# Kernel optimization log

Measured on AMD Instinct MI355X. Metric: run time of the kernel, lower is better.

The kernel has to match this reference:

```python
import math
import jax, jax.numpy as jnp
import numpy as np

B, T, DIM, H = 2, 2048, 2048, 16
D = DIM // H  # head_dim = 128


def setup_inputs() -> dict:
    key = jax.random.key(0)
    ks = jax.random.split(key, 6)
    s = 0.02
    x = jax.random.normal(ks[0], (B, T, DIM), dtype=jnp.float32)
    # causal mask: True = keep, False = masked (matches masked_fill(mask==0, -inf))
    attn_mask = jnp.tril(jnp.ones((T, T), dtype=bool))[None, None, :, :]
    Wq = jax.random.normal(ks[1], (DIM, DIM), dtype=jnp.float32) * s
    Wk = jax.random.normal(ks[2], (DIM, D), dtype=jnp.float32) * s
    Wv = jax.random.normal(ks[3], (DIM, D), dtype=jnp.float32) * s
    Wo = jax.random.normal(ks[4], (DIM, DIM), dtype=jnp.float32) * s
    return {
        "x": x, "attn_mask": attn_mask,
        "Wq": Wq, "bq": jnp.zeros((DIM,), jnp.float32),
        "Wk": Wk, "bk": jnp.zeros((D,), jnp.float32),
        "Wv": Wv, "bv": jnp.zeros((D,), jnp.float32),
        "Wo": Wo, "bo": jnp.zeros((DIM,), jnp.float32),
    }


def _rope_freqs(t_len, d):
    inv_freq = 1.0 / (10000.0 ** (jnp.arange(0, d, 2, dtype=jnp.float32) / d))
    f = jnp.arange(t_len, dtype=jnp.float32)[:, None] * inv_freq[None, :]  # [T, d/2]
    # duplicate to full head dim so cos/sin align with rotate_half's half split
    cos = jnp.concatenate([jnp.cos(f), jnp.cos(f)], axis=-1)[None, None]  # [1,1,T,d]
    sin = jnp.concatenate([jnp.sin(f), jnp.sin(f)], axis=-1)[None, None]
    return cos, sin


def _rotate_half(u):
    d2 = u.shape[-1] // 2
    return jnp.concatenate([-u[..., d2:], u[..., :d2]], axis=-1)


def reference(x, attn_mask, Wq, bq, Wk, bk, Wv, bv, Wo, bo):
    Bx, Tx, C = x.shape
    q = (x @ Wq + bq).reshape(Bx, Tx, H, D).transpose(0, 2, 1, 3)  # [B,H,T,D]
    k = (x @ Wk + bk)[:, None]  # [B,1,T,D] single shared KV head (MQA)
    v = (x @ Wv + bv)[:, None]
    cos, sin = _rope_freqs(Tx, D)
    q = q * cos + _rotate_half(q) * sin
    k = k * cos + _rotate_half(k) * sin
    attn = jnp.matmul(q, k.swapaxes(-2, -1)) / math.sqrt(D)  # [B,H,T,T]
    attn = jnp.where(attn_mask, attn, jnp.float32(-jnp.inf))
    attn = jax.nn.softmax(attn, axis=-1)
    out = jnp.matmul(attn, v)  # [B,H,T,D]
    out = out.transpose(0, 2, 1, 3).reshape(Bx, Tx, C)
    return out @ Wo + bo
```

## Files before the change

kernel.cpp:

```cpp
#include <hip/hip_runtime.h>

typedef unsigned short u16;
typedef unsigned int u32;
typedef __bf16 bf16x8 __attribute__((ext_vector_type(8)));
typedef float f32x4 __attribute__((ext_vector_type(4)));
typedef float f32x16 __attribute__((ext_vector_type(16)));
typedef u32 u32x4 __attribute__((ext_vector_type(4)));

__device__ __forceinline__ u16 bfu(float x) {
  union { __bf16 h; u16 u; } z; z.h = (__bf16)x; return z.u;
}
__device__ __forceinline__ u32 pk2(float a, float b) {
  union { __bf16 h[2]; u32 u; } z;
  z.h[0] = (__bf16)a; z.h[1] = (__bf16)b;
  return z.u;
}
__device__ __forceinline__ void gl_lds16(const u16* g, u16* l) {
  __builtin_amdgcn_global_load_lds((const __attribute__((address_space(1))) void*)g,
                                   (__attribute__((address_space(3))) void*)l, 16, 0, 0);
}

__global__ __launch_bounds__(256) void cvt_bf16(const float* __restrict__ src, u16* __restrict__ dst, int n8) {
  int i = blockIdx.x * 256 + threadIdx.x;
  if (i >= n8) return;
  const float4* s4 = (const float4*)src;
  float4 a = s4[2 * i], b = s4[2 * i + 1];
  u32x4 o;
  o[0] = pk2(a.x, a.y); o[1] = pk2(a.z, a.w);
  o[2] = pk2(b.x, b.y); o[3] = pk2(b.z, b.w);
  ((u32x4*)dst)[i] = o;
}

__global__ void transpose_cvt(const float* __restrict__ src, u16* __restrict__ dst, int R, int C) {
  __shared__ float tile[32][33];
  const int c0 = blockIdx.x * 32, r0 = blockIdx.y * 32;
  const int tx = threadIdx.x, ty = threadIdx.y;
#pragma unroll
  for (int i = 0; i < 4; ++i)
    tile[ty + i * 8][tx] = src[(size_t)(r0 + ty + i * 8) * C + c0 + tx];
  __syncthreads();
#pragma unroll
  for (int i = 0; i < 4; ++i)
    dst[(size_t)(c0 + ty + i * 8) * R + r0 + tx] = bfu(tile[tx][ty + i * 8]);
}

__global__ void transpose_v(const float* __restrict__ QKV, const float* __restrict__ bv, u16* __restrict__ Vt) {
  __shared__ float tile[32][33];
  const int t0 = blockIdx.x * 32, d0 = blockIdx.y * 32, b = blockIdx.z;
  const int tx = threadIdx.x, ty = threadIdx.y;
#pragma unroll
  for (int i = 0; i < 4; ++i)
    tile[ty + i * 8][tx] = QKV[(size_t)(b * 2048 + t0 + ty + i * 8) * 2304 + 2176 + d0 + tx] + bv[d0 + tx];
  __syncthreads();
#pragma unroll
  for (int i = 0; i < 4; ++i)
    Vt[(size_t)b * 262144 + (size_t)(d0 + ty + i * 8) * 2048 + t0 + tx] = bfu(tile[tx][ty + i * 8]);
}

__global__ __launch_bounds__(256) void rope_qk(const float* __restrict__ QKV, const float* __restrict__ bq,
                                               const float* __restrict__ bk,
                                               u16* __restrict__ Qb, u16* __restrict__ Kb) {
  const int row = blockIdx.x;
  const int b = row >> 11, t = row & 2047;
  const int tid = threadIdx.x;
  const float* qrow = QKV + (size_t)row * 2304;
  const float scale = 0.1275173862437171f;
  const float nl2 = -0.20762050593046f;
#pragma unroll
  for (int it = 0; it < 4; ++it) {
    int idx = tid + it * 256;
    int h = idx >> 6, j = idx & 63;
    float q0 = qrow[h * 128 + j] + bq[h * 128 + j];
    float q1 = qrow[h * 128 + j + 64] + bq[h * 128 + j + 64];
    float ang = (float)t * exp2f((float)j * nl2);
    float s = sinf(ang), c = cosf(ang);
    size_t o = ((size_t)((b * 16 + h) * 2048 + t)) * 128 + j;
    Qb[o]      = bfu((q0 * c - q1 * s) * scale);
    Qb[o + 64] = bfu((q1 * c + q0 * s) * scale);
  }
  if (tid < 64) {
    int j = tid;
    float k0 = qrow[2048 + j] + bk[j];
    float k1 = qrow[2048 + j + 64] + bk[j + 64];
    float ang = (float)t * exp2f((float)j * nl2);
    float s = sinf(ang), c = cosf(ang);
    size_t o = (size_t)row * 128 + j;
    Kb[o]      = bfu(k0 * c - k1 * s);
    Kb[o + 64] = bfu(k1 * c + k0 * s);
  }
}

template <bool BIAS>
__global__ __launch_bounds__(256) void gemm_bt(const u16* __restrict__ A, const u16* __restrict__ Bt,
                                               const float* __restrict__ bias, float* __restrict__ C,
                                               int M, int N, int K) {
  const int n0 = blockIdx.x * 128, m0 = blockIdx.y * 128;
  const int tid = threadIdx.x, lane = tid & 63;
  const int wid = tid >> 6, wr = wid >> 1, wc = wid & 1;
  __shared__ __align__(16) u16 As[128 * 32];
  __shared__ __align__(16) u16 Bs[128 * 32];
  f32x4 acc[4][4];
#pragma unroll
  for (int i = 0; i < 4; ++i)
#pragma unroll
    for (int j = 0; j < 4; ++j)
#pragma unroll
      for (int rr = 0; rr < 4; ++rr) acc[i][j][rr] = 0.f;

  const int c0 = tid, c1 = tid + 256;
  const int ar0 = c0 >> 2, ac0 = (c0 & 3) * 8;
  const int ar1 = c1 >> 2, ac1 = (c1 & 3) * 8;
  const int r = lane & 15, g = lane >> 4;

  for (int k0 = 0; k0 < K; k0 += 32) {
    gl_lds16(A + (size_t)(m0 + ar0) * K + k0 + ac0, As + c0 * 8);
    gl_lds16(A + (size_t)(m0 + ar1) * K + k0 + ac1, As + c1 * 8);
    gl_lds16(Bt + (size_t)(n0 + ar0) * K + k0 + ac0, Bs + c0 * 8);
    gl_lds16(Bt + (size_t)(n0 + ar1) * K + k0 + ac1, Bs + c1 * 8);
    __syncthreads();
    bf16x8 af[4], bfr[4];
#pragma unroll
    for (int mi = 0; mi < 4; ++mi)
      af[mi] = *reinterpret_cast<const bf16x8*>(&As[(wr * 64 + mi * 16 + r) * 32 + g * 8]);
#pragma unroll
    for (int ni = 0; ni < 4; ++ni)
      bfr[ni] = *reinterpret_cast<const bf16x8*>(&Bs[(wc * 64 + ni * 16 + r) * 32 + g * 8]);
#pragma unroll
    for (int mi = 0; mi < 4; ++mi)
#pragma unroll
      for (int ni = 0; ni < 4; ++ni)
        acc[mi][ni] = __builtin_amdgcn_mfma_f32_16x16x32_bf16(af[mi], bfr[ni], acc[mi][ni], 0, 0, 0);
    __syncthreads();
  }
#pragma unroll
  for (int mi = 0; mi < 4; ++mi)
#pragma unroll
    for (int ni = 0; ni < 4; ++ni) {
      int col = n0 + wc * 64 + ni * 16 + r;
      float bia = BIAS ? bias[col] : 0.f;
#pragma unroll
      for (int reg = 0; reg < 4; ++reg) {
        int row = m0 + wr * 64 + mi * 16 + g * 4 + reg;
        C[(size_t)row * N + col] = acc[mi][ni][reg] + bia;
      }
    }
}

__global__ __launch_bounds__(256, 2) void attn_kernel(const u16* __restrict__ Qb, const u16* __restrict__ Kb,
                                                      const u16* __restrict__ Vt, u16* __restrict__ Ob) {
  const int bid = blockIdx.x;
  const int grp = bid >> 5;
  const int chunk = (bid < 256) ? (15 - grp) : (grp - 8);
  const int bh = bid & 31, h = bh & 15, b = bh >> 4;
  const int tid = threadIdx.x, wid = tid >> 6, lane = tid & 63;
  const int l31 = lane & 31, hf = lane >> 5;

  __shared__ __align__(16) u16 smem[32768];
  u16* Ksb = smem;
  u16* Vsb = smem + 16384;

  const u16* Kbase = Kb + (size_t)b * 2048 * 128;
  const u16* Vbase = Vt + (size_t)b * 128 * 2048;

  int krow[4], kcol[4], vrow[4], vcol[4];
#pragma unroll
  for (int i = 0; i < 4; ++i) {
    const int seg = wid * 4 + i;
    const int r = seg * 4 + (lane >> 4);
    krow[i] = r; kcol[i] = (((lane & 15) ^ (r & 15)) << 3);
    const int d = seg * 8 + (lane >> 3);
    vrow[i] = d; vcol[i] = (((lane & 7) ^ (d & 7)) << 3);
  }
  const int ldsoff = wid * 2048 + lane * 8;

#define STAGE(buf, kvb_) do {                                                              \
    _Pragma("unroll") for (int i_ = 0; i_ < 4; ++i_)                                       \
      gl_lds16(Kbase + (size_t)((kvb_) + krow[i_]) * 128 + kcol[i_],                       \
               &Ksb[(buf) * 8192 + ldsoff + i_ * 512]);                                    \
    _Pragma("unroll") for (int i_ = 0; i_ < 4; ++i_)                                       \
      gl_lds16(Vbase + (size_t)vrow[i_] * 2048 + (kvb_) + vcol[i_],                        \
               &Vsb[(buf) * 8192 + ldsoff + i_ * 512]);                                    \
  } while (0)

  const int xk16 = l31 & 15;
  const int xk8 = l31 & 7;

  const int cb = chunk * 128;
  const int qw = cb + wid * 32;
  const u16* qptr = Qb + ((size_t)((b * 16 + h) * 2048 + qw + l31)) * 128;
  bf16x8 qf[8];
#pragma unroll
  for (int c = 0; c < 8; ++c)
    qf[c] = *reinterpret_cast<const bf16x8*>(qptr + c * 16 + hf * 8);

  f32x16 ot[4];
#pragma unroll
  for (int dt = 0; dt < 4; ++dt)
#pragma unroll
    for (int rr = 0; rr < 16; ++rr) ot[dt][rr] = 0.f;
  float m = -1e30f, lsum = 0.f;

  const int nkv = 2 * chunk + 2;
  STAGE(0, 0);
  for (int it = 0; it < nkv; ++it) {
    const int kvb = it << 6, cur = it & 1;
    if (it + 1 < nkv) {
      STAGE(cur ^ 1, kvb + 64);
      asm volatile("s_waitcnt vmcnt(8)" ::: "memory");
    } else {
      asm volatile("s_waitcnt vmcnt(0)" ::: "memory");
    }
    __builtin_amdgcn_s_barrier();

    if (kvb <= qw) {
      const u16* ks = Ksb + cur * 8192;
      const u16* vs = Vsb + cur * 8192;
      f32x16 st0, st1;
#pragma unroll
      for (int rr = 0; rr < 16; ++rr) { st0[rr] = 0.f; st1[rr] = -1e30f; }
      const u16* ksr0 = ks + l31 * 128;
#pragma unroll
      for (int c = 0; c < 8; ++c) {
        bf16x8 kf = *reinterpret_cast<const bf16x8*>(ksr0 + (((2 * c + hf) ^ xk16) << 3));
        st0 = __builtin_amdgcn_mfma_f32_32x32x16_bf16(kf, qf[c], st0, 0, 0, 0);
      }
      const bool a1 = (kvb + 32 <= qw);
      if (a1) {
#pragma unroll
        for (int rr = 0; rr < 16; ++rr) st1[rr] = 0.f;
        const u16* ksr1 = ks + (32 + l31) * 128;
#pragma unroll
        for (int c = 0; c < 8; ++c) {
          bf16x8 kf = *reinterpret_cast<const bf16x8*>(ksr1 + (((2 * c + hf) ^ xk16) << 3));
          st1 = __builtin_amdgcn_mfma_f32_32x32x16_bf16(kf, qf[c], st1, 0, 0, 0);
        }
        if (kvb + 32 == qw) {
#pragma unroll
          for (int rr = 0; rr < 16; ++rr) {
            int kvl = (rr & 3) + 8 * (rr >> 2) + 4 * hf;
            if (kvl > l31) st1[rr] = -1e30f;
          }
        }
      }
      if (kvb == qw) {
#pragma unroll
        for (int rr = 0; rr < 16; ++rr) {
          int kvl = (rr & 3) + 8 * (rr >> 2) + 4 * hf;
          if (kvl > l31) st0[rr] = -1e30f;
        }
      }

      float tmax = st0[0];
#pragma unroll
      for (int rr = 1; rr < 16; ++rr) tmax = fmaxf(tmax, st0[rr]);
#pragma unroll
      for (int rr = 0; rr < 16; ++rr) tmax = fmaxf(tmax, st1[rr]);
      tmax = fmaxf(tmax, __shfl_xor(tmax, 32, 64));
      if (!__all(tmax - m <= 8.f)) {
        const float mnew = fmaxf(m, tmax);
        const float alpha = exp2f(m - mnew);
        lsum *= alpha;
#pragma unroll
        for (int dt = 0; dt < 4; ++dt)
#pragma unroll
          for (int rr = 0; rr < 16; ++rr) ot[dt][rr] *= alpha;
        m = mnew;
      }
      float rsum = 0.f;
#pragma unroll
      for (int rr = 0; rr < 16; ++rr) { st0[rr] = exp2f(st0[rr] - m); rsum += st0[rr]; }
#pragma unroll
      for (int rr = 0; rr < 16; ++rr) { st1[rr] = exp2f(st1[rr] - m); rsum += st1[rr]; }
      rsum += __shfl_xor(rsum, 32, 64);
      lsum += rsum;

#pragma unroll
      for (int n = 0; n < 2; ++n) {
        if (n == 1 && !a1) break;
        const f32x16& pp = n ? st1 : st0;
#pragma unroll
        for (int s = 0; s < 2; ++s) {
          u32 a0p = pk2(pp[8 * s + 0], pp[8 * s + 1]);
          u32 a1p = pk2(pp[8 * s + 2], pp[8 * s + 3]);
          u32 b0p = pk2(pp[8 * s + 4], pp[8 * s + 5]);
          u32 b1p = pk2(pp[8 * s + 6], pp[8 * s + 7]);
          u32 k0 = hf ? b0p : a0p, k1 = hf ? b1p : a1p;
          u32 sd0 = hf ? a0p : b0p, sd1 = hf ? a1p : b1p;
          u32 r0 = (u32)__shfl_xor((int)sd0, 32, 64);
          u32 r1 = (u32)__shfl_xor((int)sd1, 32, 64);
          u32x4 pw;
          pw[0] = hf ? r0 : k0; pw[1] = hf ? r1 : k1;
          pw[2] = hf ? k0 : r0; pw[3] = hf ? k1 : r1;
          bf16x8 pb = __builtin_bit_cast(bf16x8, pw);
          const int cc = n * 4 + s * 2 + hf;
#pragma unroll
          for (int dt = 0; dt < 4; ++dt) {
            bf16x8 vf = *reinterpret_cast<const bf16x8*>(
                &vs[(dt * 32 + l31) * 64 + ((cc ^ xk8) << 3)]);
            ot[dt] = __builtin_amdgcn_mfma_f32_32x32x16_bf16(vf, pb, ot[dt], 0, 0, 0);
          }
        }
      }
    }
    __builtin_amdgcn_s_barrier();
  }

  u16* myt = smem + wid * (32 * 136);
  const float inv = 1.f / lsum;
#pragma unroll
  for (int dt = 0; dt < 4; ++dt)
#pragma unroll
    for (int rq = 0; rq < 4; ++rq) {
      int d = dt * 32 + 8 * rq + 4 * hf;
      u32 lo = pk2(ot[dt][rq * 4 + 0] * inv, ot[dt][rq * 4 + 1] * inv);
      u32 hi = pk2(ot[dt][rq * 4 + 2] * inv, ot[dt][rq * 4 + 3] * inv);
      u32* dstp = (u32*)&myt[l31 * 136 + d];
      dstp[0] = lo; dstp[1] = hi;
    }
  __syncthreads();
  const size_t outbase = ((size_t)(b * 2048 + qw)) * 2048 + h * 128;
#pragma unroll
  for (int i = 0; i < 8; ++i) {
    int chunk2 = i * 64 + lane;
    int row = chunk2 >> 4, c16 = chunk2 & 15;
    u32x4 v = *reinterpret_cast<const u32x4*>(&myt[row * 136 + c16 * 8]);
    *reinterpret_cast<u32x4*>(Ob + outbase + (size_t)row * 2048 + c16 * 8) = v;
  }
#undef STAGE
}

extern "C" void kernel_launch(void* const* d_in, const int* in_sizes, int n_in,
                              void* d_out, int out_size, void* d_ws, size_t ws_size,
                              hipStream_t stream) {
  const float* x  = (const float*)d_in[0];
  const float* Wq = (const float*)d_in[2];
  const float* bq = (const float*)d_in[3];
  const float* Wk = (const float*)d_in[4];
  const float* bk = (const float*)d_in[5];
  const float* Wv = (const float*)d_in[6];
  const float* bv = (const float*)d_in[7];
  const float* Wo = (const float*)d_in[8];
  const float* bo = (const float*)d_in[9];

  char* ws = (char*)d_ws;
  u16*  xb    = (u16*)ws;   ws += (size_t)4096 * 2048 * 2;
  u16*  WqkvT = (u16*)ws;   ws += (size_t)2304 * 2048 * 2;
  u16*  WoT   = (u16*)ws;   ws += (size_t)2048 * 2048 * 2;
  float* QKV  = (float*)ws; ws += (size_t)4096 * 2304 * 4;
  u16*  Qb    = (u16*)ws;   ws += (size_t)2 * 16 * 2048 * 128 * 2;
  u16*  Kb    = (u16*)ws;   ws += (size_t)2 * 2048 * 128 * 2;
  u16*  Vt    = (u16*)ws;   ws += (size_t)2 * 128 * 2048 * 2;
  u16*  Ob    = (u16*)ws;   ws += (size_t)4096 * 2048 * 2;

  dim3 tb(32, 8);
  cvt_bf16<<<4096, 256, 0, stream>>>(x, xb, 1048576);
  transpose_cvt<<<dim3(64, 64), tb, 0, stream>>>(Wq, WqkvT, 2048, 2048);
  transpose_cvt<<<dim3(4, 64),  tb, 0, stream>>>(Wk, WqkvT + (size_t)2048 * 2048, 2048, 128);
  transpose_cvt<<<dim3(4, 64),  tb, 0, stream>>>(Wv, WqkvT + (size_t)2176 * 2048, 2048, 128);
  transpose_cvt<<<dim3(64, 64), tb, 0, stream>>>(Wo, WoT, 2048, 2048);

  gemm_bt<false><<<dim3(18, 32), 256, 0, stream>>>(xb, WqkvT, nullptr, QKV, 4096, 2304, 2048);
  rope_qk<<<4096, 256, 0, stream>>>(QKV, bq, bk, Qb, Kb);
  transpose_v<<<dim3(64, 4, 2), tb, 0, stream>>>(QKV, bv, Vt);
  attn_kernel<<<512, 256, 0, stream>>>(Qb, Kb, Vt, Ob);
  gemm_bt<true><<<dim3(16, 32), 256, 0, stream>>>(Ob, WoT, bo, (float*)d_out, 4096, 2048, 2048);
}
```

Measured before the change: 230.0 us.

## Load K/V fragments directly from global memory into registers, dropping LDS staging

The attention kernel no longer stages K and V tiles in double-buffered shared memory with block-wide barriers. Each wave now loads its K and V MFMA fragments straight from global memory into registers and runs only as many KV tiles as its own query rows need, so waves iterate independently. This removes the barriers and LDS traffic but gives up cross-wave data sharing, so each of the four waves re-reads the same K/V from global/L2. It also raises register pressure from the 16 K fragments and 16 V fragments held per iteration.

```diff
diff --git a/kernel.cpp b/kernel.cpp
--- a/kernel.cpp
+++ b/kernel.cpp
@@ -155,38 +155,12 @@
   const int tid = threadIdx.x, wid = tid >> 6, lane = tid & 63;
   const int l31 = lane & 31, hf = lane >> 5;
 
-  __shared__ __align__(16) u16 smem[32768];
-  u16* Ksb = smem;
-  u16* Vsb = smem + 16384;
+  __shared__ __align__(16) u16 otile[4][32 * 136];
 
   const u16* Kbase = Kb + (size_t)b * 2048 * 128;
   const u16* Vbase = Vt + (size_t)b * 128 * 2048;
 
-  int krow[4], kcol[4], vrow[4], vcol[4];
-#pragma unroll
-  for (int i = 0; i < 4; ++i) {
-    const int seg = wid * 4 + i;
-    const int r = seg * 4 + (lane >> 4);
-    krow[i] = r; kcol[i] = (((lane & 15) ^ (r & 15)) << 3);
-    const int d = seg * 8 + (lane >> 3);
-    vrow[i] = d; vcol[i] = (((lane & 7) ^ (d & 7)) << 3);
-  }
-  const int ldsoff = wid * 2048 + lane * 8;
-
-#define STAGE(buf, kvb_) do {                                                              \
-    _Pragma("unroll") for (int i_ = 0; i_ < 4; ++i_)                                       \
-      gl_lds16(Kbase + (size_t)((kvb_) + krow[i_]) * 128 + kcol[i_],                       \
-               &Ksb[(buf) * 8192 + ldsoff + i_ * 512]);                                    \
-    _Pragma("unroll") for (int i_ = 0; i_ < 4; ++i_)                                       \
-      gl_lds16(Vbase + (size_t)vrow[i_] * 2048 + (kvb_) + vcol[i_],                        \
-               &Vsb[(buf) * 8192 + ldsoff + i_ * 512]);                                    \
-  } while (0)
-
-  const int xk16 = l31 & 15;
-  const int xk8 = l31 & 7;
-
-  const int cb = chunk * 128;
-  const int qw = cb + wid * 32;
+  const int qw = chunk * 128 + wid * 32;
   const u16* qptr = Qb + ((size_t)((b * 16 + h) * 2048 + qw + l31)) * 128;
   bf16x8 qf[8];
 #pragma unroll
@@ -200,112 +174,105 @@
     for (int rr = 0; rr < 16; ++rr) ot[dt][rr] = 0.f;
   float m = -1e30f, lsum = 0.f;
 
-  const int nkv = 2 * chunk + 2;
-  STAGE(0, 0);
-  for (int it = 0; it < nkv; ++it) {
-    const int kvb = it << 6, cur = it & 1;
-    if (it + 1 < nkv) {
-      STAGE(cur ^ 1, kvb + 64);
-      asm volatile("s_waitcnt vmcnt(8)" ::: "memory");
-    } else {
-      asm volatile("s_waitcnt vmcnt(0)" ::: "memory");
-    }
-    __builtin_amdgcn_s_barrier();
-
-    if (kvb <= qw) {
-      const u16* ks = Ksb + cur * 8192;
-      const u16* vs = Vsb + cur * 8192;
-      f32x16 st0, st1;
-#pragma unroll
-      for (int rr = 0; rr < 16; ++rr) { st0[rr] = 0.f; st1[rr] = -1e30f; }
-      const u16* ksr0 = ks + l31 * 128;
-#pragma unroll
-      for (int c = 0; c < 8; ++c) {
-        bf16x8 kf = *reinterpret_cast<const bf16x8*>(ksr0 + (((2 * c + hf) ^ xk16) << 3));
-        st0 = __builtin_amdgcn_mfma_f32_32x32x16_bf16(kf, qf[c], st0, 0, 0, 0);
-      }
-      const bool a1 = (kvb + 32 <= qw);
-      if (a1) {
-#pragma unroll
-        for (int rr = 0; rr < 16; ++rr) st1[rr] = 0.f;
-        const u16* ksr1 = ks + (32 + l31) * 128;
-#pragma unroll
-        for (int c = 0; c < 8; ++c) {
-          bf16x8 kf = *reinterpret_cast<const bf16x8*>(ksr1 + (((2 * c + hf) ^ xk16) << 3));
-          st1 = __builtin_amdgcn_mfma_f32_32x32x16_bf16(kf, qf[c], st1, 0, 0, 0);
-        }
-        if (kvb + 32 == qw) {
-#pragma unroll
-          for (int rr = 0; rr < 16; ++rr) {
-            int kvl = (rr & 3) + 8 * (rr >> 2) + 4 * hf;
-            if (kvl > l31) st1[rr] = -1e30f;
-          }
+  const int nt = (qw >> 6) + 1;
+  for (int it = 0; it < nt; ++it) {
+    const int kvb = it << 6;
+    const u16* k0p = Kbase + (size_t)(kvb + l31) * 128 + hf * 8;
+    const u16* k1p = k0p + 32 * 128;
+    bf16x8 kf0[8], kf1[8];
+#pragma unroll
+    for (int c = 0; c < 8; ++c) kf0[c] = *reinterpret_cast<const bf16x8*>(k0p + c * 16);
+#pragma unroll
+    for (int c = 0; c < 8; ++c) kf1[c] = *reinterpret_cast<const bf16x8*>(k1p + c * 16);
+
+    f32x16 st0, st1;
+#pragma unroll
+    for (int rr = 0; rr < 16; ++rr) { st0[rr] = 0.f; st1[rr] = -1e30f; }
+#pragma unroll
+    for (int c = 0; c < 8; ++c)
+      st0 = __builtin_amdgcn_mfma_f32_32x32x16_bf16(kf0[c], qf[c], st0, 0, 0, 0);
+    const bool a1 = (kvb + 32 <= qw);
+    if (a1) {
+#pragma unroll
+      for (int rr = 0; rr < 16; ++rr) st1[rr] = 0.f;
+#pragma unroll
+      for (int c = 0; c < 8; ++c)
+        st1 = __builtin_amdgcn_mfma_f32_32x32x16_bf16(kf1[c], qf[c], st1, 0, 0, 0);
+      if (kvb + 32 == qw) {
+#pragma unroll
+        for (int rr = 0; rr < 16; ++rr) {
+          int kvl = (rr & 3) + 8 * (rr >> 2) + 4 * hf;
+          if (kvl > l31) st1[rr] = -1e30f;
         }
       }
-      if (kvb == qw) {
-#pragma unroll
-        for (int rr = 0; rr < 16; ++rr) {
-          int kvl = (rr & 3) + 8 * (rr >> 2) + 4 * hf;
-          if (kvl > l31) st0[rr] = -1e30f;
-        }
+    }
+    if (kvb == qw) {
+#pragma unroll
+      for (int rr = 0; rr < 16; ++rr) {
+        int kvl = (rr & 3) + 8 * (rr >> 2) + 4 * hf;
+        if (kvl > l31) st0[rr] = -1e30f;
       }
-
-      float tmax = st0[0];
-#pragma unroll
-      for (int rr = 1; rr < 16; ++rr) tmax = fmaxf(tmax, st0[rr]);
-#pragma unroll
-      for (int rr = 0; rr < 16; ++rr) tmax = fmaxf(tmax, st1[rr]);
-      tmax = fmaxf(tmax, __shfl_xor(tmax, 32, 64));
-      if (!__all(tmax - m <= 8.f)) {
-        const float mnew = fmaxf(m, tmax);
-        const float alpha = exp2f(m - mnew);
-        lsum *= alpha;
+    }
+
+    bf16x8 vf[4][4];
+#pragma unroll
+    for (int cc = 0; cc < 4; ++cc)
+#pragma unroll
+      for (int dt = 0; dt < 4; ++dt)
+        vf[cc][dt] = *reinterpret_cast<const bf16x8*>(
+            Vbase + (size_t)(dt * 32 + l31) * 2048 + kvb + cc * 16 + hf * 8);
+
+    float tmax = st0[0];
+#pragma unroll
+    for (int rr = 1; rr < 16; ++rr) tmax = fmaxf(tmax, st0[rr]);
+#pragma unroll
+    for (int rr = 0; rr < 16; ++rr) tmax = fmaxf(tmax, st1[rr]);
+    tmax = fmaxf(tmax, __shfl_xor(tmax, 32, 64));
+    if (!__all(tmax - m <= 8.f)) {
+      const float mnew = fmaxf(m, tmax);
+      const float alpha = exp2f(m - mnew);
+      lsum *= alpha;
+#pragma unroll
+      for (int dt = 0; dt < 4; ++dt)
+#pragma unroll
+        for (int rr = 0; rr < 16; ++rr) ot[dt][rr] *= alpha;
+      m = mnew;
+    }
+    float rsum = 0.f;
+#pragma unroll
+    for (int rr = 0; rr < 16; ++rr) { st0[rr] = exp2f(st0[rr] - m); rsum += st0[rr]; }
+#pragma unroll
+    for (int rr = 0; rr < 16; ++rr) { st1[rr] = exp2f(st1[rr] - m); rsum += st1[rr]; }
+    rsum += __shfl_xor(rsum, 32, 64);
+    lsum += rsum;
+
+#pragma unroll
+    for (int n = 0; n < 2; ++n) {
+      if (n == 1 && !a1) break;
+      const f32x16& pp = n ? st1 : st0;
+#pragma unroll
+      for (int s = 0; s < 2; ++s) {
+        u32 a0p = pk2(pp[8 * s + 0], pp[8 * s + 1]);
+        u32 a1p = pk2(pp[8 * s + 2], pp[8 * s + 3]);
+        u32 b0p = pk2(pp[8 * s + 4], pp[8 * s + 5]);
+        u32 b1p = pk2(pp[8 * s + 6], pp[8 * s + 7]);
+        u32 k0 = hf ? b0p : a0p, k1 = hf ? b1p : a1p;
+        u32 sd0 = hf ? a0p : b0p, sd1 = hf ? a1p : b1p;
+        u32 r0 = (u32)__shfl_xor((int)sd0, 32, 64);
+        u32 r1 = (u32)__shfl_xor((int)sd1, 32, 64);
+        u32x4 pw;
+        pw[0] = hf ? r0 : k0; pw[1] = hf ? r1 : k1;
+        pw[2] = hf ? k0 : r0; pw[3] = hf ? k1 : r1;
+        bf16x8 pb = __builtin_bit_cast(bf16x8, pw);
+        const int cc = n * 2 + s;
 #pragma unroll
         for (int dt = 0; dt < 4; ++dt)
-#pragma unroll
-          for (int rr = 0; rr < 16; ++rr) ot[dt][rr] *= alpha;
-        m = mnew;
+          ot[dt] = __builtin_amdgcn_mfma_f32_32x32x16_bf16(vf[cc][dt], pb, ot[dt], 0, 0, 0);
       }
-      float rsum = 0.f;
-#pragma unroll
-      for (int rr = 0; rr < 16; ++rr) { st0[rr] = exp2f(st0[rr] - m); rsum += st0[rr]; }
-#pragma unroll
-      for (int rr = 0; rr < 16; ++rr) { st1[rr] = exp2f(st1[rr] - m); rsum += st1[rr]; }
-      rsum += __shfl_xor(rsum, 32, 64);
-      lsum += rsum;
-
-#pragma unroll
-      for (int n = 0; n < 2; ++n) {
-        if (n == 1 && !a1) break;
-        const f32x16& pp = n ? st1 : st0;
-#pragma unroll
-        for (int s = 0; s < 2; ++s) {
-          u32 a0p = pk2(pp[8 * s + 0], pp[8 * s + 1]);
-          u32 a1p = pk2(pp[8 * s + 2], pp[8 * s + 3]);
-          u32 b0p = pk2(pp[8 * s + 4], pp[8 * s + 5]);
-          u32 b1p = pk2(pp[8 * s + 6], pp[8 * s + 7]);
-          u32 k0 = hf ? b0p : a0p, k1 = hf ? b1p : a1p;
-          u32 sd0 = hf ? a0p : b0p, sd1 = hf ? a1p : b1p;
-          u32 r0 = (u32)__shfl_xor((int)sd0, 32, 64);
-          u32 r1 = (u32)__shfl_xor((int)sd1, 32, 64);
-          u32x4 pw;
-          pw[0] = hf ? r0 : k0; pw[1] = hf ? r1 : k1;
-          pw[2] = hf ? k0 : r0; pw[3] = hf ? k1 : r1;
-          bf16x8 pb = __builtin_bit_cast(bf16x8, pw);
-          const int cc = n * 4 + s * 2 + hf;
-#pragma unroll
-          for (int dt = 0; dt < 4; ++dt) {
-            bf16x8 vf = *reinterpret_cast<const bf16x8*>(
-                &vs[(dt * 32 + l31) * 64 + ((cc ^ xk8) << 3)]);
-            ot[dt] = __builtin_amdgcn_mfma_f32_32x32x16_bf16(vf, pb, ot[dt], 0, 0, 0);
-          }
-        }
-      }
-    }
-    __builtin_amdgcn_s_barrier();
-  }
-
-  u16* myt = smem + wid * (32 * 136);
+    }
+  }
+
+  u16* myt = otile[wid];
   const float inv = 1.f / lsum;
 #pragma unroll
   for (int dt = 0; dt < 4; ++dt)
@@ -326,7 +293,6 @@
     u32x4 v = *reinterpret_cast<const u32x4*>(&myt[row * 136 + c16 * 8]);
     *reinterpret_cast<u32x4*>(Ob + outbase + (size_t)row * 2048 + c16 * 8) = v;
   }
-#undef STAGE
 }
 
 extern "C" void kernel_launch(void* const* d_in, const int* in_sizes, int n_in,
```

Result: slower. 296.8 us (+29.1%).

## Fuse bias, RoPE and bf16 conversion into the QKV projection GEMM epilogue

Applied to the files above, without the earlier changes.

Adds a dedicated QKV GEMM whose waves each own 32 rows by all 128 columns of a tile, so every lane holds both halves of each head dimension pair. The epilogue applies bias, RoPE rotation and the softmax scale for Q and K and writes bf16 directly, and writes V as row-major bf16 that a smaller transpose kernel then converts to Vt. This removes the fp32 QKV intermediate (about 38MB written and re-read) and the separate rope kernel launch. In exchange the epilogue uses __sincosf, a lower-accuracy intrinsic, makes scattered 2-byte stores, and the GEMM tile shape changes from 2x2 warps to 4x1.

```diff
diff --git a/kernel.cpp b/kernel.cpp
--- a/kernel.cpp
+++ b/kernel.cpp
@@ -44,49 +44,103 @@
     dst[(size_t)(c0 + ty + i * 8) * R + r0 + tx] = bfu(tile[tx][ty + i * 8]);
 }
 
-__global__ void transpose_v(const float* __restrict__ QKV, const float* __restrict__ bv, u16* __restrict__ Vt) {
-  __shared__ float tile[32][33];
+__global__ void transpose_v16(const u16* __restrict__ Vrow, u16* __restrict__ Vt) {
+  __shared__ u16 tile[32][33];
   const int t0 = blockIdx.x * 32, d0 = blockIdx.y * 32, b = blockIdx.z;
   const int tx = threadIdx.x, ty = threadIdx.y;
 #pragma unroll
   for (int i = 0; i < 4; ++i)
-    tile[ty + i * 8][tx] = QKV[(size_t)(b * 2048 + t0 + ty + i * 8) * 2304 + 2176 + d0 + tx] + bv[d0 + tx];
+    tile[ty + i * 8][tx] = Vrow[(size_t)(b * 2048 + t0 + ty + i * 8) * 128 + d0 + tx];
   __syncthreads();
 #pragma unroll
   for (int i = 0; i < 4; ++i)
-    Vt[(size_t)b * 262144 + (size_t)(d0 + ty + i * 8) * 2048 + t0 + tx] = bfu(tile[tx][ty + i * 8]);
-}
-
-__global__ __launch_bounds__(256) void rope_qk(const float* __restrict__ QKV, const float* __restrict__ bq,
-                                               const float* __restrict__ bk,
-                                               u16* __restrict__ Qb, u16* __restrict__ Kb) {
-  const int row = blockIdx.x;
-  const int b = row >> 11, t = row & 2047;
-  const int tid = threadIdx.x;
-  const float* qrow = QKV + (size_t)row * 2304;
-  const float scale = 0.1275173862437171f;
+    Vt[(size_t)b * 262144 + (size_t)(d0 + ty + i * 8) * 2048 + t0 + tx] = tile[tx][ty + i * 8];
+}
+
+__global__ __launch_bounds__(256) void gemm_qkv(const u16* __restrict__ A, const u16* __restrict__ Bt,
+                                                const float* __restrict__ bq, const float* __restrict__ bk,
+                                                const float* __restrict__ bv,
+                                                u16* __restrict__ Qb, u16* __restrict__ Kb,
+                                                u16* __restrict__ Vrow) {
+  const int nt = blockIdx.x;
+  const int n0 = nt * 128, m0 = blockIdx.y * 128;
+  const int K = 2048;
+  const int tid = threadIdx.x, lane = tid & 63;
+  const int wid = tid >> 6;
+  __shared__ __align__(16) u16 As[128 * 32];
+  __shared__ __align__(16) u16 Bs[128 * 32];
+  f32x4 acc[2][8];
+#pragma unroll
+  for (int i = 0; i < 2; ++i)
+#pragma unroll
+    for (int j = 0; j < 8; ++j)
+#pragma unroll
+      for (int rr = 0; rr < 4; ++rr) acc[i][j][rr] = 0.f;
+
+  const int c0 = tid, c1 = tid + 256;
+  const int ar0 = c0 >> 2, ac0 = (c0 & 3) * 8;
+  const int ar1 = c1 >> 2, ac1 = (c1 & 3) * 8;
+  const int r = lane & 15, g = lane >> 4;
+
+  for (int k0 = 0; k0 < K; k0 += 32) {
+    gl_lds16(A + (size_t)(m0 + ar0) * K + k0 + ac0, As + c0 * 8);
+    gl_lds16(A + (size_t)(m0 + ar1) * K + k0 + ac1, As + c1 * 8);
+    gl_lds16(Bt + (size_t)(n0 + ar0) * K + k0 + ac0, Bs + c0 * 8);
+    gl_lds16(Bt + (size_t)(n0 + ar1) * K + k0 + ac1, Bs + c1 * 8);
+    __syncthreads();
+    bf16x8 af[2], bfr[8];
+#pragma unroll
+    for (int mi = 0; mi < 2; ++mi)
+      af[mi] = *reinterpret_cast<const bf16x8*>(&As[(wid * 32 + mi * 16 + r) * 32 + g * 8]);
+#pragma unroll
+    for (int ni = 0; ni < 8; ++ni)
+      bfr[ni] = *reinterpret_cast<const bf16x8*>(&Bs[(ni * 16 + r) * 32 + g * 8]);
+#pragma unroll
+    for (int mi = 0; mi < 2; ++mi)
+#pragma unroll
+      for (int ni = 0; ni < 8; ++ni)
+        acc[mi][ni] = __builtin_amdgcn_mfma_f32_16x16x32_bf16(af[mi], bfr[ni], acc[mi][ni], 0, 0, 0);
+    __syncthreads();
+  }
+
   const float nl2 = -0.20762050593046f;
-#pragma unroll
-  for (int it = 0; it < 4; ++it) {
-    int idx = tid + it * 256;
-    int h = idx >> 6, j = idx & 63;
-    float q0 = qrow[h * 128 + j] + bq[h * 128 + j];
-    float q1 = qrow[h * 128 + j + 64] + bq[h * 128 + j + 64];
-    float ang = (float)t * exp2f((float)j * nl2);
-    float s = sinf(ang), c = cosf(ang);
-    size_t o = ((size_t)((b * 16 + h) * 2048 + t)) * 128 + j;
-    Qb[o]      = bfu((q0 * c - q1 * s) * scale);
-    Qb[o + 64] = bfu((q1 * c + q0 * s) * scale);
-  }
-  if (tid < 64) {
-    int j = tid;
-    float k0 = qrow[2048 + j] + bk[j];
-    float k1 = qrow[2048 + j + 64] + bk[j + 64];
-    float ang = (float)t * exp2f((float)j * nl2);
-    float s = sinf(ang), c = cosf(ang);
-    size_t o = (size_t)row * 128 + j;
-    Kb[o]      = bfu(k0 * c - k1 * s);
-    Kb[o + 64] = bfu(k1 * c + k0 * s);
+  if (nt < 17) {
+    const bool isQ = (nt < 16);
+    const float sc = isQ ? 0.1275173862437171f : 1.0f;
+    const float* bias = isQ ? (bq + nt * 128) : bk;
+    u16* dst = isQ ? Qb : Kb;
+#pragma unroll
+    for (int mi = 0; mi < 2; ++mi)
+#pragma unroll
+      for (int reg = 0; reg < 4; ++reg) {
+        const int row = m0 + wid * 32 + mi * 16 + g * 4 + reg;
+        const int b = row >> 11, t = row & 2047;
+#pragma unroll
+        for (int ni = 0; ni < 4; ++ni) {
+          const int j = ni * 16 + r;
+          const float v0 = acc[mi][ni][reg] + bias[j];
+          const float v1 = acc[mi][ni + 4][reg] + bias[j + 64];
+          const float ang = (float)t * exp2f((float)j * nl2);
+          float s, c;
+          __sincosf(ang, &s, &c);
+          const size_t base = isQ ? (((size_t)((b * 16 + nt) * 2048 + t)) * 128 + j)
+                                  : (((size_t)(b * 2048 + t)) * 128 + j);
+          dst[base]      = bfu((v0 * c - v1 * s) * sc);
+          dst[base + 64] = bfu((v1 * c + v0 * s) * sc);
+        }
+      }
+  } else {
+#pragma unroll
+    for (int mi = 0; mi < 2; ++mi)
+#pragma unroll
+      for (int reg = 0; reg < 4; ++reg) {
+        const int row = m0 + wid * 32 + mi * 16 + g * 4 + reg;
+#pragma unroll
+        for (int ni = 0; ni < 8; ++ni) {
+          const int d = ni * 16 + r;
+          Vrow[(size_t)row * 128 + d] = bfu(acc[mi][ni][reg] + bv[d]);
+        }
+      }
   }
 }
 
@@ -346,9 +400,9 @@
   u16*  xb    = (u16*)ws;   ws += (size_t)4096 * 2048 * 2;
   u16*  WqkvT = (u16*)ws;   ws += (size_t)2304 * 2048 * 2;
   u16*  WoT   = (u16*)ws;   ws += (size_t)2048 * 2048 * 2;
-  float* QKV  = (float*)ws; ws += (size_t)4096 * 2304 * 4;
   u16*  Qb    = (u16*)ws;   ws += (size_t)2 * 16 * 2048 * 128 * 2;
   u16*  Kb    = (u16*)ws;   ws += (size_t)2 * 2048 * 128 * 2;
+  u16*  Vrow  = (u16*)ws;   ws += (size_t)2 * 2048 * 128 * 2;
   u16*  Vt    = (u16*)ws;   ws += (size_t)2 * 128 * 2048 * 2;
   u16*  Ob    = (u16*)ws;   ws += (size_t)4096 * 2048 * 2;
 
@@ -359,9 +413,8 @@
   transpose_cvt<<<dim3(4, 64),  tb, 0, stream>>>(Wv, WqkvT + (size_t)2176 * 2048, 2048, 128);
   transpose_cvt<<<dim3(64, 64), tb, 0, stream>>>(Wo, WoT, 2048, 2048);
 
-  gemm_bt<false><<<dim3(18, 32), 256, 0, stream>>>(xb, WqkvT, nullptr, QKV, 4096, 2304, 2048);
-  rope_qk<<<4096, 256, 0, stream>>>(QKV, bq, bk, Qb, Kb);
-  transpose_v<<<dim3(64, 4, 2), tb, 0, stream>>>(QKV, bv, Vt);
+  gemm_qkv<<<dim3(18, 32), 256, 0, stream>>>(xb, WqkvT, bq, bk, bv, Qb, Kb, Vrow);
+  transpose_v16<<<dim3(64, 4, 2), tb, 0, stream>>>(Vrow, Vt);
   attn_kernel<<<512, 256, 0, stream>>>(Qb, Kb, Vt, Ob);
   gemm_bt<true><<<dim3(16, 32), 256, 0, stream>>>(Ob, WoT, bo, (float*)d_out, 4096, 2048, 2048);
 }
```

Result: slower. 240.8 us (+4.7%).
